# Performance work log

Hardware: AMD Instinct MI355X
Metric: run time of the kernel (lower is better)

## Reference

```python
import math
import jax, jax.numpy as jnp
import numpy as np

NUM_HEADS = 8
TEMPORAL_DECAY = 0.1


def setup_inputs() -> dict:
    key = jax.random.key(0)
    ks = jax.random.split(key, 12)
    B, N, D = 2, 2048, 512
    H = NUM_HEADS
    s = 0.02
    inp = {
        "node_features": jax.random.normal(ks[0], (B, N, D), dtype=jnp.float32),
        "adjacency": jax.random.randint(ks[1], (B, N, N), 0, 2, dtype=jnp.int32),
        "edge_times": jax.random.uniform(ks[2], (B, N, N), dtype=jnp.float32),
        "current_time": 2,
        "wq": jax.random.normal(ks[3], (D, D), dtype=jnp.float32) * s,
        "bq": jnp.zeros((D,), dtype=jnp.float32),
        "wk": jax.random.normal(ks[4], (D, D), dtype=jnp.float32) * s,
        "bk": jnp.zeros((D,), dtype=jnp.float32),
        "wv": jax.random.normal(ks[5], (D, D), dtype=jnp.float32) * s,
        "bv": jnp.zeros((D,), dtype=jnp.float32),
        "wo": jax.random.normal(ks[6], (D, D), dtype=jnp.float32) * s,
        "bo": jnp.zeros((D,), dtype=jnp.float32),
        "wt": jax.random.normal(ks[7], (H, 1), dtype=jnp.float32) * s,  # time_proj: Linear(1, H)
        "bt": jnp.zeros((H,), dtype=jnp.float32),
    }
    return inp


def reference(node_features, adjacency, edge_times, current_time,
              wq, bq, wk, bk, wv, bv, wo, bo, wt, bt):
    B, N, D = node_features.shape
    H = NUM_HEADS
    dk = D // H

    def proj(w, b):
        # (B,N,D) -> (B,H,N,dk)
        return (node_features @ w.T + b).reshape(B, N, H, dk).transpose(0, 2, 1, 3)

    q = proj(wq, bq)
    k = proj(wk, bk)
    v = proj(wv, bv)

    # scaled dot-product scores: (B,H,N,N)
    attn = jnp.einsum("bhnd,bhmd->bhnm", q, k) / math.sqrt(dk)

    # adjacency mask (zero entries -> -inf)
    graph_mask = (adjacency == 0)[:, None, :, :]  # (B,1,N,N)
    attn = jnp.where(graph_mask, -jnp.inf, attn)

    # temporal-decay bias: Linear(1, H) applied to exp(-decay * dt), permuted to (B,H,N,N)
    time_diff = jnp.maximum(jnp.float32(current_time) - edge_times, 0.0)  # (B,N,N)
    temporal_weight = jnp.exp(-TEMPORAL_DECAY * time_diff)  # (B,N,N)
    temporal_bias = (temporal_weight[:, None, :, :] * wt[:, 0][None, :, None, None]
                     + bt[None, :, None, None])  # (B,H,N,N)
    attn = attn + temporal_bias

    attn = jax.nn.softmax(attn, axis=-1)  # dropout rate is 0.0

    out = jnp.einsum("bhnm,bhmd->bhnd", attn, v)  # (B,H,N,dk)
    out = out.transpose(0, 2, 1, 3).reshape(B, N, D)
    out = out @ wo.T + bo
    return node_features + out
```

## Files before the change

kernel.cpp:

```cpp
#include <hip/hip_runtime.h>

#define BB 2
#define NN 2048
#define DD 512
#define HH 8
#define DK 64

#define LOG2E 1.44269504f
#define SCL2  0.18033688f

typedef __attribute__((ext_vector_type(4))) float f32x4;
typedef __attribute__((ext_vector_type(16))) float f32x16;
typedef __attribute__((ext_vector_type(8))) short bf16x8;
typedef __attribute__((ext_vector_type(2))) int i32x2;
typedef __attribute__((ext_vector_type(4))) int i32x4;

__device__ __forceinline__ short f2bf(float f) {
  union { float f; unsigned u; } v; v.f = f;
  unsigned r = v.u + 0x7fffu + ((v.u >> 16) & 1u);
  return (short)(r >> 16);
}

__device__ __forceinline__ bf16x8 pack8(float4 a, float4 b) {
  bf16x8 r;
  r[0] = f2bf(a.x); r[1] = f2bf(a.y); r[2] = f2bf(a.z); r[3] = f2bf(a.w);
  r[4] = f2bf(b.x); r[5] = f2bf(b.y); r[6] = f2bf(b.z); r[7] = f2bf(b.w);
  return r;
}

#define WAITV(n) do { asm volatile("s_waitcnt vmcnt(" #n ")" ::: "memory"); \
                      __builtin_amdgcn_sched_barrier(0); } while (0)
#define GLOAD_LDS(g, l) __builtin_amdgcn_global_load_lds( \
    (const __attribute__((address_space(1))) void*)(g),   \
    (__attribute__((address_space(3))) void*)(l), 16, 0, 0)
#define SBAR() asm volatile("s_barrier" ::: "memory")
#define LDM(d, o) asm volatile("global_load_dwordx2 %0, %1, off offset:" o \
                               : "=v"(d) : "v"(mrowp))
#define CVTPK(d, a, b) asm("v_cvt_pk_bf16_f32 %0, %1, %2" : "=v"(d) : "v"(a), "v"(b))
#define PLSWAP(a, b) asm("v_permlane32_swap_b32 %0, %1" : "+v"(a), "+v"(b))

__global__ __launch_bounds__(256) void prep(
    const int* __restrict__ adj, const float* __restrict__ et,
    const int* __restrict__ ctp, short* __restrict__ M,
    const float* __restrict__ X,
    const float* __restrict__ wq, const float* __restrict__ wk,
    const float* __restrict__ wv, const float* __restrict__ wo,
    short* __restrict__ Xb, short* __restrict__ Wb)
{
  const float ct = (float)(*ctp);
  const float kd = -0.1f * LOG2E;
  const size_t base = ((size_t)blockIdx.x * 256 + threadIdx.x) * 8;
  const size_t stride = (size_t)2048 * 256 * 8;
#pragma unroll
  for (int it = 0; it < 2; it++) {
    const size_t i = base + (size_t)it * stride;
    int4 a0 = *(const int4*)(adj + i);
    int4 a1 = *(const int4*)(adj + i + 4);
    float4 e0 = *(const float4*)(et + i);
    float4 e1 = *(const float4*)(et + i + 4);
    const int av[8] = {a0.x, a0.y, a0.z, a0.w, a1.x, a1.y, a1.z, a1.w};
    const float ev[8] = {e0.x, e0.y, e0.z, e0.w, e1.x, e1.y, e1.z, e1.w};
    bf16x8 r;
#pragma unroll
    for (int j = 0; j < 8; j++) {
      const float tv = (av[j] == 0) ? -1.f : exp2f(kd * fmaxf(ct - ev[j], 0.f));
      r[j] = f2bf(tv);
    }
    *(bf16x8*)(M + i) = r;
  }
  if (blockIdx.x < 1536) {
    const size_t XN = (size_t)4096 * DD;
    const size_t i = base;
    const float* src;
    short* dst;
    if (i < XN) { src = X + i; dst = Xb + i; }
    else {
      const size_t j = i - XN;
      const int sel = (int)(j >> 18);
      const size_t off = j & 262143;
      src = (sel == 0 ? wq : sel == 1 ? wk : sel == 2 ? wv : wo) + off;
      dst = Wb + j;
    }
    float4 a = *(const float4*)src;
    float4 b = *(const float4*)(src + 4);
    *(bf16x8*)dst = pack8(a, b);
  }
}

__global__ __launch_bounds__(256, 2) void qkv_gemm(
    const short* __restrict__ Xb, const short* __restrict__ Wb,
    const float* __restrict__ bq, const float* __restrict__ bk, const float* __restrict__ bv,
    short* __restrict__ qo, short* __restrict__ ko, short* __restrict__ vto)
{
  __shared__ short As[2][128 * 64];
  __shared__ short Bs[2][64 * 64];

  const int tid = threadIdx.x;
  const int lane = tid & 63;
  const int w = tid >> 6;
  const int q4 = lane >> 4;
  const int c = lane & 15;

  const int bid = blockIdx.x;
  const int mt = bid & 31;
  const int nt = bid >> 5;
  const int sel = nt >> 3;
  const int nw = (nt & 7) * 64;
  const int m0 = mt * 128;
  const short* Wm = Wb + (size_t)sel * 262144;
  const float* bias = sel == 0 ? bq : (sel == 1 ? bk : bv);
  const float oscale = (sel == 0) ? SCL2 : 1.0f;

  const int sr = lane >> 3;
  const int sc = ((lane & 7) ^ sr) * 8;
  const short* ap = Xb + (size_t)(m0 + w * 32 + sr) * DD + sc;
  const short* bp = Wm + (size_t)(nw + w * 16 + sr) * DD + sc;

  f32x4 acc[2][4];
#pragma unroll
  for (int is = 0; is < 2; is++)
#pragma unroll
    for (int ns = 0; ns < 4; ns++) acc[is][ns] = f32x4{0.f, 0.f, 0.f, 0.f};

#define QSTAGE(BUF, K0)                                                    \
  { GLOAD_LDS(ap + (K0),           &As[BUF][(w * 32 + 0) * 64]);           \
    GLOAD_LDS(ap + 8 * DD + (K0),  &As[BUF][(w * 32 + 8) * 64]);           \
    GLOAD_LDS(ap + 16 * DD + (K0), &As[BUF][(w * 32 + 16) * 64]);          \
    GLOAD_LDS(ap + 24 * DD + (K0), &As[BUF][(w * 32 + 24) * 64]);          \
    GLOAD_LDS(bp + (K0),           &Bs[BUF][(w * 16 + 0) * 64]);           \
    GLOAD_LDS(bp + 8 * DD + (K0),  &Bs[BUF][(w * 16 + 8) * 64]); }

#define QCOMPUTE(BUF)                                                            \
  { const short* Asb = &As[BUF][0];                                              \
    const short* Bsb = &Bs[BUF][0];                                              \
    _Pragma("unroll") for (int kc = 0; kc < 2; kc++) {                           \
      bf16x8 af[2], bfr[4];                                                      \
      _Pragma("unroll") for (int is = 0; is < 2; is++)                           \
        af[is] = *(const bf16x8*)&Asb[(w * 32 + is * 16 + c) * 64 +              \
                                      (((kc * 4 + q4) ^ (c & 7)) * 8)];          \
      _Pragma("unroll") for (int ns = 0; ns < 4; ns++)                           \
        bfr[ns] = *(const bf16x8*)&Bsb[(ns * 16 + c) * 64 +                      \
                                       (((kc * 4 + q4) ^ (c & 7)) * 8)];         \
      _Pragma("unroll") for (int is = 0; is < 2; is++)                           \
        _Pragma("unroll") for (int ns = 0; ns < 4; ns++)                         \
          acc[is][ns] = __builtin_amdgcn_mfma_f32_16x16x32_bf16(af[is], bfr[ns], \
                                                           acc[is][ns], 0, 0, 0); \
    } }

  QSTAGE(0, 0)
  __syncthreads();
  for (int ks = 0; ks < 8; ks++) {
    if (ks < 7) QSTAGE((ks + 1) & 1, (ks + 1) * 64)
    QCOMPUTE(ks & 1)
    __syncthreads();
  }
#undef QSTAGE
#undef QCOMPUTE

#pragma unroll
  for (int ns = 0; ns < 4; ns++) {
    const int n = nw + ns * 16 + c;
    const float bval = bias[n];
    const int hh = n >> 6, d = n & 63;
#pragma unroll
    for (int is = 0; is < 2; is++)
#pragma unroll
      for (int r = 0; r < 4; r++) {
        const int m = m0 + w * 32 + is * 16 + q4 * 4 + r;
        const int bb = m >> 11, tok = m & 2047;
        const float val = (acc[is][ns][r] + bval) * oscale;
        if (sel == 2)      vto[((size_t)(bb * HH + hh) * DK + d) * NN + tok] = f2bf(val);
        else if (sel == 1) ko [((size_t)(bb * HH + hh) * NN + tok) * DK + d] = f2bf(val);
        else               qo [((size_t)(bb * HH + hh) * NN + tok) * DK + d] = f2bf(val);
      }
  }
}

__global__ __launch_bounds__(256, 2) void attn_kernel(
    const short* __restrict__ qt, const short* __restrict__ kt, const short* __restrict__ vtt,
    const short* __restrict__ M,
    const float* __restrict__ wt,
    short* __restrict__ po_out, float* __restrict__ pl_out)
{
  __shared__ short Ks[2][64 * 64];
  __shared__ short Vs[2][64 * 64];

  const int tid = threadIdx.x;
  const int lane = tid & 63;
  const int w = tid >> 6;
  const int l31 = lane & 31;
  const int hi = lane >> 5;
  const int l7 = l31 & 7;

  const int bid = blockIdx.x;
  const int xcd = bid & 7;
  const int b = xcd >> 2;
  const int jsp = xcd & 3;
  const int rest = bid >> 3;
  const int h = rest & 7;
  const int qblk = rest >> 3;
  const int i0w = qblk * 128 + w * 32;
  const int jbase = jsp * 512;

  const float wth2 = wt[h] * LOG2E;

  const short* qb = qt + ((size_t)(b * HH + h) * NN + i0w) * DK;
  const short* kb = kt + (size_t)(b * HH + h) * NN * DK;
  const short* vb = vtt + (size_t)(b * HH + h) * DK * NN;
  const short* mrowp = M + ((size_t)b * NN + i0w + l31) * NN + jbase + hi * 4;

  bf16x8 aq[4];
#pragma unroll
  for (int kc = 0; kc < 4; kc++)
    aq[kc] = *(const bf16x8*)(qb + l31 * DK + kc * 16 + hi * 8);
  asm volatile("" :: "v"(aq[0]), "v"(aq[1]), "v"(aq[2]), "v"(aq[3]), "v"(wth2));
  WAITV(0);

  unsigned ka[4], va[4];
#pragma unroll
  for (int kc = 0; kc < 4; kc++)
    ka[kc] = (unsigned)(l31 * 128 + (((kc * 2 + hi) ^ l7) * 16));
#pragma unroll
  for (int jc = 0; jc < 4; jc++) {
    const int js = jc >> 1, ch = jc & 1;
    va[jc] = (unsigned)(l31 * 128 + (((js * 4 + ch * 2 + hi) ^ l7) * 16));
  }

  float lp = 0.f;
  f32x16 oacc[2];
#pragma unroll
  for (int ds = 0; ds < 2; ds++)
#pragma unroll
    for (int r = 0; r < 16; r++) oacc[ds][r] = 0.f;

  const int srow = lane >> 3;
  const int ssw = ((lane & 7) ^ srow) * 8;
  const short* kp0 = kb + (size_t)(jbase + w * 16 + srow) * DK + ssw;
  const short* kp1 = kp0 + 8 * DK;
  const short* vp0 = vb + (size_t)(w * 16 + srow) * NN + jbase + ssw;
  const short* vp1 = vp0 + 8 * NN;
  const char* KsB = (const char*)&Ks[0][0];
  const char* VsB = (const char*)&Vs[0][0];

#define STAGE(BUFN)                                                        \
  { GLOAD_LDS(kp0, &Ks[BUFN][(w * 16) * 64]);                              \
    GLOAD_LDS(kp1, &Ks[BUFN][(w * 16 + 8) * 64]);                          \
    GLOAD_LDS(vp0, &Vs[BUFN][(w * 16) * 64]);                              \
    GLOAD_LDS(vp1, &Vs[BUFN][(w * 16 + 8) * 64]);                          \
    __builtin_amdgcn_sched_barrier(0); }

#define KADV() { kp0 += 64 * DK; kp1 += 64 * DK; vp0 += 64; vp1 += 64; }
#define MADV() { mrowp += 64; }

#define ISSUE_MASK(MU)                                                     \
  { LDM(MU[0][0], "0");  LDM(MU[0][1], "16"); LDM(MU[0][2], "32");  LDM(MU[0][3], "48");  \
    LDM(MU[1][0], "64"); LDM(MU[1][1], "80"); LDM(MU[1][2], "96");  LDM(MU[1][3], "112"); \
    __builtin_amdgcn_sched_barrier(0); }

  i32x2 muA[2][4], muB[2][4];

  STAGE(0)
  KADV()
  ISSUE_MASK(muA)
  MADV()

#define COMPUTE_QK(BUFC)                                                         \
    f32x16 sacc[2];                                                              \
    __builtin_amdgcn_s_setprio(1);                                               \
    _Pragma("unroll") for (int js = 0; js < 2; js++) {                           \
      _Pragma("unroll") for (int r = 0; r < 16; r++) sacc[js][r] = 0.f;          \
      _Pragma("unroll") for (int kc = 0; kc < 4; kc++) {                         \
        bf16x8 kf = *(const bf16x8*)(KsB + (BUFC) * 8192 + js * 4096 + ka[kc]);  \
        sacc[js] = __builtin_amdgcn_mfma_f32_32x32x16_bf16(kf, aq[kc],           \
                                                           sacc[js], 0, 0, 0);   \
      }                                                                          \
    }                                                                            \
    __builtin_amdgcn_s_setprio(0);

#define COMPUTE_SM_PV(BUFC, MU)                                                  \
    __builtin_amdgcn_s_setprio(1);                                               \
    _Pragma("unroll") for (int js = 0; js < 2; js++) {                           \
      float p[16];                                                               \
      _Pragma("unroll") for (int r = 0; r < 16; r++) {                           \
        const int dw = ((r & 3) < 2) ? MU[js][r >> 2][0] : MU[js][r >> 2][1];    \
        union { float f; unsigned u; } tu;                                       \
        tu.u = (r & 1) ? ((unsigned)dw & 0xffff0000u) : ((unsigned)dw << 16);    \
        const float tv = tu.f;                                                   \
        const float pp = exp2f(fmaf(tv, wth2, sacc[js][r]));                     \
        p[r] = (tv < 0.f) ? 0.f : pp;                                            \
        lp += p[r];                                                              \
      }                                                                          \
      bf16x8 pf[2];                                                              \
      _Pragma("unroll") for (int ch = 0; ch < 2; ch++) {                         \
        const int rb = ch * 8;                                                   \
        int w0, w1, w2, w3;                                                      \
        CVTPK(w0, p[rb + 0], p[rb + 1]);                                         \
        CVTPK(w1, p[rb + 2], p[rb + 3]);                                         \
        CVTPK(w2, p[rb + 4], p[rb + 5]);                                         \
        CVTPK(w3, p[rb + 6], p[rb + 7]);                                         \
        PLSWAP(w0, w2);                                                          \
        PLSWAP(w1, w3);                                                          \
        i32x4 bi;                                                                \
        bi[0] = w0; bi[1] = w1; bi[2] = w2; bi[3] = w3;                          \
        union { i32x4 i; bf16x8 h; } cv; cv.i = bi;                              \
        pf[ch] = cv.h;                                                           \
      }                                                                          \
      _Pragma("unroll") for (int ds = 0; ds < 2; ds++) {                         \
        _Pragma("unroll") for (int ch = 0; ch < 2; ch++) {                       \
          bf16x8 vf = *(const bf16x8*)(VsB + (BUFC) * 8192 + ds * 4096 +         \
                                       va[js * 2 + ch]);                         \
          oacc[ds] = __builtin_amdgcn_mfma_f32_32x32x16_bf16(vf, pf[ch],         \
                                                             oacc[ds], 0, 0, 0); \
        }                                                                        \
      }                                                                          \
    }                                                                            \
    __builtin_amdgcn_s_setprio(0);

#define ATTN_ITER(T, MUC, MUN)                                                   \
  {                                                                              \
    STAGE(((T) + 1) & 1)                        \
    KADV()                                                                       \
    WAITV(12);                                   \
    SBAR();                                                                      \
    COMPUTE_QK((T) & 1)                                                          \
    ISSUE_MASK(MUN)                             \
    MADV()                                                                       \
    WAITV(12);                                   \
    COMPUTE_SM_PV((T) & 1, MUC)                                                  \
    SBAR();                                                                      \
  }

  for (int t2 = 0; t2 < 3; t2++) {
    ATTN_ITER(2 * t2,     muA, muB)
    ATTN_ITER(2 * t2 + 1, muB, muA)
  }
  ATTN_ITER(6, muA, muB)
  {
    WAITV(8);
    SBAR();
    COMPUTE_QK(1)
    WAITV(0);
    COMPUTE_SM_PV(1, muB)
  }

#undef ATTN_ITER
#undef COMPUTE_QK
#undef COMPUTE_SM_PV
#undef STAGE
#undef KADV
#undef MADV
#undef ISSUE_MASK

  const float lt = lp + __shfl_xor(lp, 32);
  const size_t ridx = ((size_t)(jsp * BB + b) * HH + h) * NN + i0w + l31;
  if (lane < 32) pl_out[ridx] = lt;
  short* pob = po_out + ridx * DK;
#pragma unroll
  for (int ds = 0; ds < 2; ds++)
#pragma unroll
    for (int r = 0; r < 16; r++) {
      const int d = ds * 32 + (r & 3) + 8 * (r >> 2) + 4 * hi;
      pob[d] = f2bf(oacc[ds][r]);
    }
}

__global__ __launch_bounds__(256) void combine(
    const short* __restrict__ PO, const float* __restrict__ PL,
    short* __restrict__ AO)
{
  const int g = blockIdx.x * 256 + threadIdx.x;
  const int t8 = g & 7;
  const int h  = (g >> 3) & 7;
  const int n  = (g >> 6) & 2047;
  const int b  = g >> 17;
  float acc[8] = {0.f, 0.f, 0.f, 0.f, 0.f, 0.f, 0.f, 0.f};
  float ls = 0.f;
#pragma unroll
  for (int jp = 0; jp < 4; jp++) {
    const size_t ridx = ((size_t)(jp * BB + b) * HH + h) * NN + n;
    bf16x8 v = *(const bf16x8*)(PO + ridx * DK + t8 * 8);
    ls += PL[ridx];
#pragma unroll
    for (int e = 0; e < 8; e++) {
      union { float f; unsigned u; } cv;
      cv.u = ((unsigned)(unsigned short)v[e]) << 16;
      acc[e] += cv.f;
    }
  }
  const float rl = 1.0f / ls;
  bf16x8 o;
#pragma unroll
  for (int e = 0; e < 8; e++) o[e] = f2bf(acc[e] * rl);
  *(bf16x8*)(AO + (size_t)g * 8) = o;
}

__global__ __launch_bounds__(256, 2) void out_gemm(
    const short* __restrict__ AO, const short* __restrict__ wob, const float* __restrict__ bo,
    const float* __restrict__ nf, float* __restrict__ out)
{
  __shared__ short As[2][128 * 64];
  __shared__ short Bs[2][64 * 64];

  const int tid = threadIdx.x;
  const int lane = tid & 63;
  const int w = tid >> 6;
  const int q4 = lane >> 4;
  const int c = lane & 15;

  const int bid = blockIdx.x;
  const int mt = bid & 31;
  const int n0 = (bid >> 5) * 64;
  const int m0 = mt * 128;

  const int sr = lane >> 3;
  const int sc = ((lane & 7) ^ sr) * 8;
  const short* ap = AO + (size_t)(m0 + w * 32 + sr) * DD + sc;
  const short* bp = wob + (size_t)(n0 + w * 16 + sr) * DD + sc;

  f32x4 acc[2][4];
#pragma unroll
  for (int is = 0; is < 2; is++)
#pragma unroll
    for (int ns = 0; ns < 4; ns++) acc[is][ns] = f32x4{0.f, 0.f, 0.f, 0.f};

#define OSTAGE(BUF, K0)                                                    \
  { GLOAD_LDS(ap + (K0),           &As[BUF][(w * 32 + 0) * 64]);           \
    GLOAD_LDS(ap + 8 * DD + (K0),  &As[BUF][(w * 32 + 8) * 64]);           \
    GLOAD_LDS(ap + 16 * DD + (K0), &As[BUF][(w * 32 + 16) * 64]);          \
    GLOAD_LDS(ap + 24 * DD + (K0), &As[BUF][(w * 32 + 24) * 64]);          \
    GLOAD_LDS(bp + (K0),           &Bs[BUF][(w * 16 + 0) * 64]);           \
    GLOAD_LDS(bp + 8 * DD + (K0),  &Bs[BUF][(w * 16 + 8) * 64]); }

#define OCOMPUTE(BUF)                                                            \
  { const short* Asb = &As[BUF][0];                                              \
    const short* Bsb = &Bs[BUF][0];                                              \
    _Pragma("unroll") for (int kc = 0; kc < 2; kc++) {                           \
      bf16x8 af[2], bfr[4];                                                      \
      _Pragma("unroll") for (int is = 0; is < 2; is++)                           \
        af[is] = *(const bf16x8*)&Asb[(w * 32 + is * 16 + c) * 64 +              \
                                      (((kc * 4 + q4) ^ (c & 7)) * 8)];          \
      _Pragma("unroll") for (int ns = 0; ns < 4; ns++)                           \
        bfr[ns] = *(const bf16x8*)&Bsb[(ns * 16 + c) * 64 +                      \
                                       (((kc * 4 + q4) ^ (c & 7)) * 8)];         \
      _Pragma("unroll") for (int is = 0; is < 2; is++)                           \
        _Pragma("unroll") for (int ns = 0; ns < 4; ns++)                         \
          acc[is][ns] = __builtin_amdgcn_mfma_f32_16x16x32_bf16(af[is], bfr[ns], \
                                                           acc[is][ns], 0, 0, 0); \
    } }

  OSTAGE(0, 0)
  __syncthreads();
  for (int ks = 0; ks < 8; ks++) {
    if (ks < 7) OSTAGE((ks + 1) & 1, (ks + 1) * 64)
    OCOMPUTE(ks & 1)
    __syncthreads();
  }
#undef OSTAGE
#undef OCOMPUTE

#pragma unroll
  for (int ns = 0; ns < 4; ns++) {
    const int n = n0 + ns * 16 + c;
    const float bval = bo[n];
#pragma unroll
    for (int is = 0; is < 2; is++)
#pragma unroll
      for (int r = 0; r < 4; r++) {
        const int m = m0 + w * 32 + is * 16 + q4 * 4 + r;
        out[(size_t)m * DD + n] = acc[is][ns][r] + bval + nf[(size_t)m * DD + n];
      }
  }
}

extern "C" void kernel_launch(void* const* d_in, const int* in_sizes, int n_in,
                              void* d_out, int out_size, void* d_ws, size_t ws_size,
                              hipStream_t stream) {
  const float* nf  = (const float*)d_in[0];
  const int*   adj = (const int*)d_in[1];
  const float* et  = (const float*)d_in[2];
  const int*   ct  = (const int*)d_in[3];
  const float* wq  = (const float*)d_in[4];
  const float* bq  = (const float*)d_in[5];
  const float* wk  = (const float*)d_in[6];
  const float* bk  = (const float*)d_in[7];
  const float* wv  = (const float*)d_in[8];
  const float* bv  = (const float*)d_in[9];
  const float* wo  = (const float*)d_in[10];
  const float* bo  = (const float*)d_in[11];
  const float* wt  = (const float*)d_in[12];

  const size_t SZ = (size_t)BB * HH * NN * DK;
  short* q   = (short*)d_ws;
  short* k   = q + SZ;
  short* vt  = k + SZ;
  short* ao  = vt + SZ;
  short* Mm  = ao + SZ;
  short* PO  = Mm + (size_t)BB * NN * NN;
  float* PL  = (float*)(PO + 4 * SZ);
  short* Xb  = (short*)(PL + 4 * BB * HH * NN);
  short* Wb  = Xb + (size_t)4096 * DD;

  prep<<<2048, 256, 0, stream>>>(adj, et, ct, Mm, nf, wq, wk, wv, wo, Xb, Wb);
  qkv_gemm<<<768, 256, 0, stream>>>(Xb, Wb, bq, bk, bv, q, k, vt);
  attn_kernel<<<1024, 256, 0, stream>>>(q, k, vt, Mm, wt, PO, PL);
  combine<<<1024, 256, 0, stream>>>(PO, PL, ao);
  out_gemm<<<256, 256, 0, stream>>>(ao, Wb + 3 * 262144, bo, nf, (float*)d_out);
}
```

Measured before the change: 97.30 us.

## Widen attention blocks to 8 waves and 128-key tiles per stage

The attention kernel now runs 512-thread blocks of 8 waves covering 256 query rows, and each pipeline stage loads 128 keys instead of 64. This halves the number of blocks and barrier-separated iterations, and lets more waves share each K/V tile in LDS. Each stage is split into two 64-key halves, and the mask loads for the second half are issued while the first half computes. In exchange, LDS use per block doubles and the V layout and swizzle are reworked, which risks bank conflicts, lower occupancy and fewer blocks to spread across the CUs.

```diff
diff --git a/kernel.cpp b/kernel.cpp
--- a/kernel.cpp
+++ b/kernel.cpp
@@ -176,14 +176,14 @@
   }
 }
 
-__global__ __launch_bounds__(256, 2) void attn_kernel(
+__global__ __launch_bounds__(512, 2) void attn_kernel(
     const short* __restrict__ qt, const short* __restrict__ kt, const short* __restrict__ vtt,
     const short* __restrict__ M,
     const float* __restrict__ wt,
     short* __restrict__ po_out, float* __restrict__ pl_out)
 {
-  __shared__ short Ks[2][64 * 64];
-  __shared__ short Vs[2][64 * 64];
+  __shared__ short Ks[2][128 * 64];
+  __shared__ short Vs[2][64 * 128];
 
   const int tid = threadIdx.x;
   const int lane = tid & 63;
@@ -199,7 +199,7 @@
   const int rest = bid >> 3;
   const int h = rest & 7;
   const int qblk = rest >> 3;
-  const int i0w = qblk * 128 + w * 32;
+  const int i0w = qblk * 256 + w * 32;
   const int jbase = jsp * 512;
 
   const float wth2 = wt[h] * LOG2E;
@@ -216,14 +216,15 @@
   asm volatile("" :: "v"(aq[0]), "v"(aq[1]), "v"(aq[2]), "v"(aq[3]), "v"(wth2));
   WAITV(0);
 
-  unsigned ka[4], va[4];
+  unsigned ka[4];
 #pragma unroll
   for (int kc = 0; kc < 4; kc++)
     ka[kc] = (unsigned)(l31 * 128 + (((kc * 2 + hi) ^ l7) * 16));
-#pragma unroll
-  for (int jc = 0; jc < 4; jc++) {
+  unsigned va2[8];
+#pragma unroll
+  for (int jc = 0; jc < 8; jc++) {
     const int js = jc >> 1, ch = jc & 1;
-    va[jc] = (unsigned)(l31 * 128 + (((js * 4 + ch * 2 + hi) ^ l7) * 16));
+    va2[jc] = (unsigned)(l31 * 256 + (((js * 4 + ch * 2 + hi) ^ (l31 & 15)) * 16));
   }
 
   float lp = 0.f;
@@ -233,60 +234,65 @@
 #pragma unroll
     for (int r = 0; r < 16; r++) oacc[ds][r] = 0.f;
 
-  const int srow = lane >> 3;
-  const int ssw = ((lane & 7) ^ srow) * 8;
-  const short* kp0 = kb + (size_t)(jbase + w * 16 + srow) * DK + ssw;
+  const int kr = w * 16 + (lane >> 3);
+  const short* kp0 = kb + (size_t)(jbase + kr) * DK + (((lane & 7) ^ (kr & 7)) * 8);
   const short* kp1 = kp0 + 8 * DK;
-  const short* vp0 = vb + (size_t)(w * 16 + srow) * NN + jbase + ssw;
-  const short* vp1 = vp0 + 8 * NN;
+  const int vr = w * 8 + (lane >> 4);
+  const short* vp0 = vb + (size_t)vr * NN + jbase + (((lane & 15) ^ (vr & 15)) * 8);
+  const short* vp1 = vb + (size_t)(vr + 4) * NN + jbase + (((lane & 15) ^ ((vr + 4) & 15)) * 8);
   const char* KsB = (const char*)&Ks[0][0];
   const char* VsB = (const char*)&Vs[0][0];
 
 #define STAGE(BUFN)                                                        \
   { GLOAD_LDS(kp0, &Ks[BUFN][(w * 16) * 64]);                              \
     GLOAD_LDS(kp1, &Ks[BUFN][(w * 16 + 8) * 64]);                          \
-    GLOAD_LDS(vp0, &Vs[BUFN][(w * 16) * 64]);                              \
-    GLOAD_LDS(vp1, &Vs[BUFN][(w * 16 + 8) * 64]);                          \
+    GLOAD_LDS(vp0, &Vs[BUFN][(w * 8) * 128]);                              \
+    GLOAD_LDS(vp1, &Vs[BUFN][(w * 8 + 4) * 128]);                          \
     __builtin_amdgcn_sched_barrier(0); }
 
-#define KADV() { kp0 += 64 * DK; kp1 += 64 * DK; vp0 += 64; vp1 += 64; }
-#define MADV() { mrowp += 64; }
-
-#define ISSUE_MASK(MU)                                                     \
+#define KADV() { kp0 += 128 * DK; kp1 += 128 * DK; vp0 += 128; vp1 += 128; }
+#define MADV() { mrowp += 128; }
+
+#define ISSUE_MASK_H0(MU)                                                  \
   { LDM(MU[0][0], "0");  LDM(MU[0][1], "16"); LDM(MU[0][2], "32");  LDM(MU[0][3], "48");  \
     LDM(MU[1][0], "64"); LDM(MU[1][1], "80"); LDM(MU[1][2], "96");  LDM(MU[1][3], "112"); \
     __builtin_amdgcn_sched_barrier(0); }
+#define ISSUE_MASK_H1(MU)                                                  \
+  { LDM(MU[0][0], "128"); LDM(MU[0][1], "144"); LDM(MU[0][2], "160"); LDM(MU[0][3], "176"); \
+    LDM(MU[1][0], "192"); LDM(MU[1][1], "208"); LDM(MU[1][2], "224"); LDM(MU[1][3], "240"); \
+    __builtin_amdgcn_sched_barrier(0); }
 
   i32x2 muA[2][4], muB[2][4];
 
   STAGE(0)
   KADV()
-  ISSUE_MASK(muA)
-  MADV()
-
-#define COMPUTE_QK(BUFC)                                                         \
-    f32x16 sacc[2];                                                              \
+  ISSUE_MASK_H0(muA)
+  WAITV(8);
+  SBAR();
+
+#define COMPUTE_QK(BUFC, JS0)                                                    \
     __builtin_amdgcn_s_setprio(1);                                               \
-    _Pragma("unroll") for (int js = 0; js < 2; js++) {                           \
-      _Pragma("unroll") for (int r = 0; r < 16; r++) sacc[js][r] = 0.f;          \
+    _Pragma("unroll") for (int jj = 0; jj < 2; jj++) {                           \
+      _Pragma("unroll") for (int r = 0; r < 16; r++) sacc[jj][r] = 0.f;          \
       _Pragma("unroll") for (int kc = 0; kc < 4; kc++) {                         \
-        bf16x8 kf = *(const bf16x8*)(KsB + (BUFC) * 8192 + js * 4096 + ka[kc]);  \
-        sacc[js] = __builtin_amdgcn_mfma_f32_32x32x16_bf16(kf, aq[kc],           \
-                                                           sacc[js], 0, 0, 0);   \
+        bf16x8 kf = *(const bf16x8*)(KsB + (BUFC) * 16384 +                      \
+                                     ((JS0) + jj) * 4096 + ka[kc]);              \
+        sacc[jj] = __builtin_amdgcn_mfma_f32_32x32x16_bf16(kf, aq[kc],           \
+                                                           sacc[jj], 0, 0, 0);   \
       }                                                                          \
     }                                                                            \
     __builtin_amdgcn_s_setprio(0);
 
-#define COMPUTE_SM_PV(BUFC, MU)                                                  \
+#define COMPUTE_SM_PV(BUFC, MU, JS0)                                             \
     __builtin_amdgcn_s_setprio(1);                                               \
-    _Pragma("unroll") for (int js = 0; js < 2; js++) {                           \
+    _Pragma("unroll") for (int jj = 0; jj < 2; jj++) {                           \
       float p[16];                                                               \
       _Pragma("unroll") for (int r = 0; r < 16; r++) {                           \
-        const int dw = ((r & 3) < 2) ? MU[js][r >> 2][0] : MU[js][r >> 2][1];    \
+        const int dw = ((r & 3) < 2) ? MU[jj][r >> 2][0] : MU[jj][r >> 2][1];    \
         union { float f; unsigned u; } tu;                                       \
         tu.u = (r & 1) ? ((unsigned)dw & 0xffff0000u) : ((unsigned)dw << 16);    \
         const float tv = tu.f;                                                   \
-        const float pp = exp2f(fmaf(tv, wth2, sacc[js][r]));                     \
+        const float pp = exp2f(fmaf(tv, wth2, sacc[jj][r]));                     \
         p[r] = (tv < 0.f) ? 0.f : pp;                                            \
         lp += p[r];                                                              \
       }                                                                          \
@@ -307,8 +313,8 @@
       }                                                                          \
       _Pragma("unroll") for (int ds = 0; ds < 2; ds++) {                         \
         _Pragma("unroll") for (int ch = 0; ch < 2; ch++) {                       \
-          bf16x8 vf = *(const bf16x8*)(VsB + (BUFC) * 8192 + ds * 4096 +         \
-                                       va[js * 2 + ch]);                         \
+          bf16x8 vf = *(const bf16x8*)(VsB + (BUFC) * 16384 + ds * 8192 +        \
+                                       va2[((JS0) + jj) * 2 + ch]);              \
           oacc[ds] = __builtin_amdgcn_mfma_f32_32x32x16_bf16(vf, pf[ch],         \
                                                              oacc[ds], 0, 0, 0); \
         }                                                                        \
@@ -316,32 +322,25 @@
     }                                                                            \
     __builtin_amdgcn_s_setprio(0);
 
-#define ATTN_ITER(T, MUC, MUN)                                                   \
+#define ATTN_ITER(T, LASTI)                                                      \
   {                                                                              \
-    STAGE(((T) + 1) & 1)                        \
-    KADV()                                                                       \
-    WAITV(12);                                   \
-    SBAR();                                                                      \
-    COMPUTE_QK((T) & 1)                                                          \
-    ISSUE_MASK(MUN)                             \
-    MADV()                                                                       \
-    WAITV(12);                                   \
-    COMPUTE_SM_PV((T) & 1, MUC)                                                  \
-    SBAR();                                                                      \
-  }
-
-  for (int t2 = 0; t2 < 3; t2++) {
-    ATTN_ITER(2 * t2,     muA, muB)
-    ATTN_ITER(2 * t2 + 1, muB, muA)
-  }
-  ATTN_ITER(6, muA, muB)
-  {
-    WAITV(8);
-    SBAR();
-    COMPUTE_QK(1)
-    WAITV(0);
-    COMPUTE_SM_PV(1, muB)
-  }
+    f32x16 sacc[2];                                                              \
+    if (!(LASTI)) { STAGE(((T) + 1) & 1) KADV() }              \
+    COMPUTE_QK((T) & 1, 0)                                                       \
+    ISSUE_MASK_H1(muB)                  \
+    if (LASTI) { WAITV(8); } else { WAITV(12); }                  \
+    COMPUTE_SM_PV((T) & 1, muA, 0)                                               \
+    COMPUTE_QK((T) & 1, 2)                                                       \
+    if (!(LASTI)) { MADV() ISSUE_MASK_H0(muA) }        \
+    if (LASTI) { WAITV(0); } else { WAITV(8); }               \
+    COMPUTE_SM_PV((T) & 1, muB, 2)                                               \
+    if (!(LASTI)) { SBAR(); }                                                    \
+  }
+
+  ATTN_ITER(0, 0)
+  ATTN_ITER(1, 0)
+  ATTN_ITER(2, 0)
+  ATTN_ITER(3, 1)
 
 #undef ATTN_ITER
 #undef COMPUTE_QK
@@ -349,7 +348,8 @@
 #undef STAGE
 #undef KADV
 #undef MADV
-#undef ISSUE_MASK
+#undef ISSUE_MASK_H0
+#undef ISSUE_MASK_H1
 
   const float lt = lp + __shfl_xor(lp, 32);
   const size_t ridx = ((size_t)(jsp * BB + b) * HH + h) * NN + i0w + l31;
@@ -502,7 +502,7 @@
 
   prep<<<2048, 256, 0, stream>>>(adj, et, ct, Mm, nf, wq, wk, wv, wo, Xb, Wb);
   qkv_gemm<<<768, 256, 0, stream>>>(Xb, Wb, bq, bk, bv, q, k, vt);
-  attn_kernel<<<1024, 256, 0, stream>>>(q, k, vt, Mm, wt, PO, PL);
+  attn_kernel<<<512, 512, 0, stream>>>(q, k, vt, Mm, wt, PO, PL);
   combine<<<1024, 256, 0, stream>>>(PO, PL, ao);
   out_gemm<<<256, 256, 0, stream>>>(ao, Wb + 3 * 262144, bo, nf, (float*)d_out);
 }
```

Measured after the change: 95.77 us. About the same (-1.6%).
